# Kernel optimization log

Hardware: AMD Instinct MI355X
Metric: run time of the kernel (lower is better)

Reference implementation:

```python
import jax, jax.numpy as jnp
import numpy as np

VOL_SHAPE = (160, 192, 160)

def setup_inputs() -> dict:
    key = jax.random.key(0)
    k1, k2 = jax.random.split(key)
    vol = jax.random.normal(k1, (2, *VOL_SHAPE, 1), dtype=jnp.float32)
    trf = jax.random.normal(k2, (2, *VOL_SHAPE, 3), dtype=jnp.float32)
    return {"vol": vol, "trf": trf}

def _warp(vol, trf):
    # vol: [B, X, Y, Z, C]; trf: [B, X, Y, Z, 3] dense displacement field ('ij' indexing)
    B = vol.shape[0]
    shape = vol.shape[1:-1]
    nd = len(shape)
    # sample locations = identity grid + displacement
    grid = jnp.stack(jnp.meshgrid(*[jnp.arange(s, dtype=vol.dtype) for s in shape], indexing='ij'), axis=-1)
    loc = grid[None] + trf  # [B, X, Y, Z, 3]
    max_f = jnp.array([s - 1 for s in shape], dtype=vol.dtype)
    max_i = jnp.array([s - 1 for s in shape], dtype=jnp.int32)
    # fill_value=None -> clamp to volume border (voxelmorph interpn semantics)
    loc = jnp.clip(loc, 0.0, max_f)
    loc0f = jnp.floor(loc)
    loc0 = jnp.clip(loc0f.astype(jnp.int32), 0, max_i)        # lower corner indices
    loc1 = jnp.clip(loc0 + 1, 0, max_i)                       # upper corner indices (clipped)
    d1 = loc1.astype(vol.dtype) - loc                          # weight for lower corner
    d0 = 1.0 - d1                                              # weight for upper corner
    b = jnp.arange(B)[:, None, None, None]
    out = jnp.zeros(vol.shape, dtype=vol.dtype)
    for c in range(2 ** nd):                                   # 8 corners, fixed small loop
        bits = [(c >> d) & 1 for d in range(nd)]
        idx = [loc1[..., d] if bits[d] else loc0[..., d] for d in range(nd)]
        w = jnp.ones(loc.shape[:-1], dtype=vol.dtype)
        for d in range(nd):
            w = w * (d0[..., d] if bits[d] else d1[..., d])
        out = out + w[..., None] * vol[b, idx[0], idx[1], idx[2]]
    return out

def reference(vol, trf):
    return _warp(vol, trf)
```

## Files before the change

kernel.cpp:

```cpp
#include <hip/hip_runtime.h>


#define NXD 160
#define NYD 192
#define NZD 160
#define NVOX (NXD * NYD * NZD)
#define NBATCH 2

#define TXT 8
#define TYT 16
#define TZT 16
#define LXT 14
#define LYT 22
#define LZT 32
#define NROWS (LXT * LYT)
#define LDS_N (NROWS * LZT)

#define TILES_X (NXD / TXT)
#define TILES_Y (NYD / TYT)
#define TILES_Z (NZD / TZT)
#define NBLOCKS (NBATCH * TILES_X * TILES_Y * TILES_Z)

typedef float f4 __attribute__((ext_vector_type(4)));

__global__ __launch_bounds__(512, 8)
void warp3d_kernel(const float* __restrict__ vol,
                   const float* __restrict__ trf,
                   float* __restrict__ out) {
    __shared__ float tile[LDS_N];

    int bid = blockIdx.x;
    int tz = bid % TILES_Z;
    int r  = bid / TILES_Z;
    int ty = r % TILES_Y;
    int r2 = r / TILES_Y;
    int tx = r2 % TILES_X;
    int b  = r2 / TILES_X;

    int x0t = tx * TXT, y0t = ty * TYT, z0t = tz * TZT;
    int lox = min(max(x0t - 3, 0), NXD - LXT);
    int loy = min(max(y0t - 3, 0), NYD - LYT);
    int loz = min(max(z0t - 8, 0), NZD - LZT);

    const float* vb = vol + (size_t)b * NVOX;

    int t = threadIdx.x;
    int zq = t & 3;
    int yq = (t >> 2) & 15;
    int xq = t >> 6;
    int x = x0t + xq, y = y0t + yq, zb0 = z0t + zq * 4;
    size_t vox_i = (((size_t)b * NXD + x) * NYD + y) * NZD + zb0;

    const f4* trfv = (const f4*)(trf + vox_i * 3);
    f4 t0 = trfv[0], t1 = trfv[1], t2 = trfv[2];

    {
        int zi = t & 31;
        int yi = t >> 5;
        int rowoff = yi * NZD;
        const float* gbase = vb + ((size_t)(lox * NYD + loy) * NZD + loz);
#pragma unroll
        for (int it = 0; it < 20; ++it) {
            int row = it * 16 + (t >> 5);
            if (row < NROWS) {
                const float* g = gbase + rowoff + (zi ^ yi);
                __builtin_amdgcn_global_load_lds(
                    (const __attribute__((address_space(1))) void*)g,
                    (__attribute__((address_space(3))) void*)
                        &tile[(it * 16 + ((t >> 6) << 1)) * LZT],
                    4, 0, 0);
            }
            yi += 16;
            int wrap = yi >= LYT;
            rowoff += wrap ? (16 * NZD - LYT * NZD + NYD * NZD) : 16 * NZD;
            if (wrap) yi -= LYT;
        }
    }
    __syncthreads();

    float dxa[4] = {t0.x, t0.w, t1.z, t2.y};
    float dya[4] = {t0.y, t1.x, t1.w, t2.z};
    float dza[4] = {t0.z, t1.y, t2.x, t2.w};

    float res[4];
#pragma unroll
    for (int j = 0; j < 4; ++j) {
        float lx = fminf(fmaxf((float)x + dxa[j], 0.0f), (float)(NXD - 1));
        float ly = fminf(fmaxf((float)y + dya[j], 0.0f), (float)(NYD - 1));
        float lz = fminf(fmaxf((float)(zb0 + j) + dza[j], 0.0f), (float)(NZD - 1));
        float fx = floorf(lx), fy = floorf(ly), fz = floorf(lz);
        int x0 = (int)fx, y0 = (int)fy, z0 = (int)fz;
        float wx0 = fminf(fx + 1.0f, (float)(NXD - 1)) - lx;
        float wy0 = fminf(fy + 1.0f, (float)(NYD - 1)) - ly;
        float wz0 = fminf(fz + 1.0f, (float)(NZD - 1)) - lz;

        int ix = x0 - lox, iy = y0 - loy, iz = z0 - loz;
        bool ok = ((unsigned)ix <= LXT - 2) & ((unsigned)iy <= LYT - 2) &
                  ((unsigned)iz <= LZT - 2);
        int sx = ok ? ix : 0;
        int sy = ok ? iy : 0;
        int sv = ok ? iz : 0;

        int base = (sx * LYT + sy) * LZT;
        int A = base + (sv ^ sy);
        int B = base + ((sv + 1) ^ sy);
        int C = base + LZT + (sv ^ (sy + 1));
        int D = base + LZT + ((sv + 1) ^ (sy + 1));

        float v000 = tile[A],              v001 = tile[B];
        float v010 = tile[C],              v011 = tile[D];
        float v100 = tile[A + LYT * LZT],  v101 = tile[B + LYT * LZT];
        float v110 = tile[C + LYT * LZT],  v111 = tile[D + LYT * LZT];

        if (!ok) {
            int x1 = min(x0 + 1, NXD - 1);
            int y1 = min(y0 + 1, NYD - 1);
            int z1 = min(z0 + 1, NZD - 1);
            size_t o00 = (size_t)(x0 * NYD + y0) * NZD;
            size_t o01 = (size_t)(x0 * NYD + y1) * NZD;
            size_t o10 = (size_t)(x1 * NYD + y0) * NZD;
            size_t o11 = (size_t)(x1 * NYD + y1) * NZD;
            v000 = vb[o00 + z0]; v001 = vb[o00 + z1];
            v010 = vb[o01 + z0]; v011 = vb[o01 + z1];
            v100 = vb[o10 + z0]; v101 = vb[o10 + z1];
            v110 = vb[o11 + z0]; v111 = vb[o11 + z1];
        }

        float wx1 = 1.0f - wx0, wy1 = 1.0f - wy0, wz1 = 1.0f - wz0;
        res[j] = wx0 * (wy0 * (wz0 * v000 + wz1 * v001) +
                        wy1 * (wz0 * v010 + wz1 * v011)) +
                 wx1 * (wy0 * (wz0 * v100 + wz1 * v101) +
                        wy1 * (wz0 * v110 + wz1 * v111));
    }

    f4 o;
    o.x = res[0]; o.y = res[1]; o.z = res[2]; o.w = res[3];
    *(f4*)(out + vox_i) = o;
}

extern "C" void kernel_launch(void* const* d_in, const int* in_sizes, int n_in,
                              void* d_out, int out_size, void* d_ws, size_t ws_size,
                              hipStream_t stream) {
    const float* vol = (const float*)d_in[0];
    const float* trf = (const float*)d_in[1];
    float* out = (float*)d_out;

    warp3d_kernel<<<NBLOCKS, 512, 0, stream>>>(vol, trf, out);
}
```

Measured before the change: 243.7 us.

## Use 16-byte global-to-LDS loads, XCD-aware block remap, and granule swizzle

The halo tile fill now uses 16-byte global_load_lds transfers in 5 iterations instead of 4-byte transfers in 20. The LDS swizzle changes from per-element XOR to XOR of 4-float granules keyed on y, so each 16-byte chunk stays contiguous. Block IDs are also remapped so consecutive hardware blocks, which go to different XCDs, cover contiguous tiles per XCD, aiming at better L2 reuse of halo data. The occupancy hint in launch_bounds is dropped, and the coarser swizzle may raise LDS bank conflicts during the gather.

```diff
diff --git a/kernel.cpp b/kernel.cpp
--- a/kernel.cpp
+++ b/kernel.cpp
@@ -15,6 +15,7 @@
 #define LZT 32
 #define NROWS (LXT * LYT)
 #define LDS_N (NROWS * LZT)
+#define NSLOT (NROWS * 8)
 
 #define TILES_X (NXD / TXT)
 #define TILES_Y (NYD / TYT)
@@ -23,13 +24,15 @@
 
 typedef float f4 __attribute__((ext_vector_type(4)));
 
-__global__ __launch_bounds__(512, 8)
+__global__ __launch_bounds__(512)
 void warp3d_kernel(const float* __restrict__ vol,
                    const float* __restrict__ trf,
                    float* __restrict__ out) {
     __shared__ float tile[LDS_N];
 
-    int bid = blockIdx.x;
+    int bid0 = blockIdx.x;
+    int bid = (bid0 & 7) * (NBLOCKS / 8) + (bid0 >> 3);
+
     int tz = bid % TILES_Z;
     int r  = bid / TILES_Z;
     int ty = r % TILES_Y;
@@ -55,25 +58,22 @@
     f4 t0 = trfv[0], t1 = trfv[1], t2 = trfv[2];
 
     {
-        int zi = t & 31;
-        int yi = t >> 5;
-        int rowoff = yi * NZD;
         const float* gbase = vb + ((size_t)(lox * NYD + loy) * NZD + loz);
 #pragma unroll
-        for (int it = 0; it < 20; ++it) {
-            int row = it * 16 + (t >> 5);
-            if (row < NROWS) {
-                const float* g = gbase + rowoff + (zi ^ yi);
+        for (int it = 0; it < 5; ++it) {
+            int slot = it * 512 + t;
+            if (slot < NSLOT) {
+                int row = slot >> 3;
+                int zg  = (slot & 7) << 2;
+                int yi  = row % LYT;
+                int xi  = row / LYT;
+                int sz  = zg ^ ((yi & 7) << 2);
+                const float* g = gbase + (size_t)xi * (NYD * NZD) + yi * NZD + sz;
                 __builtin_amdgcn_global_load_lds(
                     (const __attribute__((address_space(1))) void*)g,
-                    (__attribute__((address_space(3))) void*)
-                        &tile[(it * 16 + ((t >> 6) << 1)) * LZT],
-                    4, 0, 0);
+                    (__attribute__((address_space(3))) void*)&tile[slot * 4],
+                    16, 0, 0);
             }
-            yi += 16;
-            int wrap = yi >= LYT;
-            rowoff += wrap ? (16 * NZD - LYT * NZD + NYD * NZD) : 16 * NZD;
-            if (wrap) yi -= LYT;
         }
     }
     __syncthreads();
@@ -102,10 +102,12 @@
         int sv = ok ? iz : 0;
 
         int base = (sx * LYT + sy) * LZT;
-        int A = base + (sv ^ sy);
-        int B = base + ((sv + 1) ^ sy);
-        int C = base + LZT + (sv ^ (sy + 1));
-        int D = base + LZT + ((sv + 1) ^ (sy + 1));
+        int sw0 = (sy & 7) << 2;
+        int sw1 = ((sy + 1) & 7) << 2;
+        int A = base + (sv ^ sw0);
+        int B = base + ((sv + 1) ^ sw0);
+        int C = base + LZT + (sv ^ sw1);
+        int D = base + LZT + ((sv + 1) ^ sw1);
 
         float v000 = tile[A],              v001 = tile[B];
         float v010 = tile[C],              v011 = tile[D];
```

New measurement: 222.1 us. 8.9% less time.
